# Kernel tuning notes

Hardware: AMD Instinct MI355X
Metric: run time of the kernel (lower is better)

Reference implementation:

```python
import jax, jax.numpy as jnp
import numpy as np

NUM_BANDS = 8
NUM_CHANNELS = 16
KC = NUM_BANDS * NUM_CHANNELS
EMA_KERNEL_LENGTH = 100
DELTA = 0.1
EPS = 1e-06
S_INIT = 0.04


def setup_inputs() -> dict:
    key = jax.random.key(0)
    kx, = jax.random.split(key, 1)
    x = jax.random.normal(kx, (32, NUM_BANDS, NUM_CHANNELS, 8192), dtype=jnp.float32)
    alpha_raw = jnp.zeros((KC,), dtype=jnp.float32)
    log_s = jnp.full((KC,), float(np.log(S_INIT / (1.0 - S_INIT))), dtype=jnp.float32)
    return {"x": x, "alpha_raw": alpha_raw, "log_s": log_s}


def _build_ema_kernel(log_s):
    # (KC, 1, L_full) causal EMA kernel, then caller slices last L taps
    Lf = EMA_KERNEL_LENGTH
    s = jax.nn.sigmoid(log_s)                      # (KC,)
    j = jnp.arange(Lf, dtype=s.dtype)              # (Lf,)
    impulse = s[:, None] * (1.0 - s[:, None]) ** j[None, :]   # (KC, Lf)
    impulse = impulse / (impulse.sum(axis=1, keepdims=True) + 1e-08)
    kernel = impulse[:, ::-1]                      # flip to causal conv kernel
    return kernel[:, None, :]                      # (KC, 1, Lf)


def reference(x, alpha_raw, log_s):
    B, K, C, T = x.shape
    x_flat = x.reshape(B, KC, T)
    alpha = jax.nn.sigmoid(alpha_raw) * 0.5        # (KC,) in (0, 0.5)
    x_mag = jnp.abs(x_flat)
    L = min(EMA_KERNEL_LENGTH, T)
    kernel = _build_ema_kernel(log_s)[:, :, -L:]   # (KC, 1, L)
    x_padded = jnp.pad(x_mag, ((0, 0), (0, 0), (L - 1, 0)))
    # depthwise causal conv: groups = KC
    M = jax.lax.conv_general_dilated(
        x_padded, kernel,
        window_strides=(1,), padding='VALID',
        feature_group_count=KC,
        dimension_numbers=('NCH', 'OIH', 'NCH'))   # (B, KC, T)
    gain = jnp.clip(M, EPS, None) ** alpha[None, :, None] + DELTA
    out_flat = x_flat / gain
    return out_flat.reshape(B, K, C, T)
```

## Files before the change

### kernel.cpp

```cpp
#include <hip/hip_runtime.h>
#include <math.h>


constexpr int T      = 8192;
constexpr int KC_    = 128;
constexpr int BLOCK  = 256;
constexpr int WPB    = BLOCK / 64;
constexpr int CHUNK  = 4;
constexpr int WELE   = 64 * CHUNK;
constexpr int WPR    = T / WELE;
constexpr int NHALO  = 25;
constexpr float EPS_   = 1e-6f;
constexpr float DELTA_ = 0.1f;
constexpr float LOG2E  = 1.4426950408889634f;

typedef float f32x4 __attribute__((ext_vector_type(4)));

__device__ __forceinline__ float fast_sigmoid(float x) {
    const float e = __builtin_amdgcn_exp2f(-x * LOG2E);
    return __builtin_amdgcn_rcpf(1.0f + e);
}

__device__ __forceinline__ float gain_div(float xv, float M, float alpha) {
    const float Mc = fmaxf(M, EPS_);
    const float g  = __builtin_amdgcn_exp2f(alpha * __builtin_amdgcn_logf(Mc)) + DELTA_;
    return xv * __builtin_amdgcn_rcpf(g);
}

__global__ __launch_bounds__(BLOCK, 8) void agc_kernel(
    const float* __restrict__ x,
    const float* __restrict__ alpha_raw,
    const float* __restrict__ log_s,
    float* __restrict__ out)
{
    __shared__ float Pe[WPB][92];

    const int tid  = threadIdx.x;
    const int lane = tid & 63;
    const int wv   = tid >> 6;
    const int gw   = blockIdx.x * WPB + wv;
    const int row  = gw / WPR;
    const int wrow = gw & (WPR - 1);
    const int kc   = row & (KC_ - 1);
    const float* __restrict__ xrow = x + (size_t)row * T;
    float* __restrict__ orow       = out + (size_t)row * T;
    const f32x4* __restrict__ x4   = reinterpret_cast<const f32x4*>(xrow);
    f32x4* __restrict__ o4         = reinterpret_cast<f32x4*>(orow);

    const int i4 = (wrow << 6) + lane;

    const f32x4 v = x4[i4];
    f32x4 pv = {0.0f, 0.0f, 0.0f, 0.0f};
    if (wrow != 0 || lane >= NHALO)
        pv = x4[i4 - NHALO];

    const float s     = fast_sigmoid(log_s[kc]);
    const float alpha = 0.5f * fast_sigmoid(alpha_raw[kc]);
    const float q     = 1.0f - s;
    const float lq    = __builtin_amdgcn_logf(q);
    const float q4    = (q * q) * (q * q);
    const float q8    = q4 * q4;
    const float q100  = __builtin_amdgcn_exp2f(100.0f * lq);
    const float norm  = (1.0f - q100) + 1e-8f;
    const float w0    = s / norm;
    const float c3    = w0 * q100;

    const float a0 = fabsf(v.x),  a1 = fabsf(v.y),  a2 = fabsf(v.z),  a3 = fabsf(v.w);
    const float b0 = fabsf(pv.x), b1 = fabsf(pv.y), b2 = fabsf(pv.z), b3 = fabsf(pv.w);

    const float pA = fmaf(q, fmaf(q, fmaf(q, a0, a1), a2), a3);
    const float pB = fmaf(q, fmaf(q, fmaf(q, b0, b1), b2), b3);

    Pe[wv][NHALO + lane] = pA;
    if (lane < NHALO) Pe[wv][lane] = pB;

    asm volatile("s_waitcnt lgkmcnt(0)" ::: "memory");

    float accE = Pe[wv][lane];
    float accO = Pe[wv][lane + 1];
    #pragma unroll
    for (int j = 2; j <= 24; j += 2) accE = fmaf(accE, q8, Pe[wv][lane + j]);
    #pragma unroll
    for (int j = 3; j <= 23; j += 2) accO = fmaf(accO, q8, Pe[wv][lane + j]);
    float M = w0 * fmaf(q4, accO, accE);

    f32x4 o;
    M = fmaf(q, M, fmaf(w0, a0, -c3 * b0));  o.x = gain_div(v.x, M, alpha);
    M = fmaf(q, M, fmaf(w0, a1, -c3 * b1));  o.y = gain_div(v.y, M, alpha);
    M = fmaf(q, M, fmaf(w0, a2, -c3 * b2));  o.z = gain_div(v.z, M, alpha);
    M = fmaf(q, M, fmaf(w0, a3, -c3 * b3));  o.w = gain_div(v.w, M, alpha);
    __builtin_nontemporal_store(o, &o4[i4]);
}

extern "C" void kernel_launch(void* const* d_in, const int* in_sizes, int n_in,
                              void* d_out, int out_size, void* d_ws, size_t ws_size,
                              hipStream_t stream) {
    const float* x         = (const float*)d_in[0];
    const float* alpha_raw = (const float*)d_in[1];
    const float* log_s     = (const float*)d_in[2];
    float* out             = (float*)d_out;
    const int nrows = in_sizes[0] / T;
    const int nblocks = nrows * (T / WELE) / WPB;
    agc_kernel<<<nblocks, BLOCK, 0, stream>>>(x, alpha_raw, log_s, out);
}
```

Baseline: 227.3 us.

## Precompute per-channel EMA constants in setup kernel and shuffle halo from registers

Adds a tiny setup kernel that computes the per-channel EMA coefficients once into workspace, so the main kernel loads them instead of recomputing sigmoid, log and exp per wave. Each lane now gets its previous-element data from a neighbouring lane through cross-lane shuffles, and only the first 25 lanes issue a second global load for the halo. This cuts redundant vector memory loads, at the cost of four shuffles per lane and an extra kernel launch with a dependency through workspace.

```diff
diff --git a/kernel.cpp b/kernel.cpp
--- a/kernel.cpp
+++ b/kernel.cpp
@@ -27,10 +27,31 @@
     return xv * __builtin_amdgcn_rcpf(g);
 }
 
+__global__ void agc_setup(const float* __restrict__ alpha_raw,
+                          const float* __restrict__ log_s,
+                          float* __restrict__ tab)
+{
+    const int kc = threadIdx.x;
+    const float s     = fast_sigmoid(log_s[kc]);
+    const float alpha = 0.5f * fast_sigmoid(alpha_raw[kc]);
+    const float q     = 1.0f - s;
+    const float lq    = __builtin_amdgcn_logf(q);
+    const float q4    = (q * q) * (q * q);
+    const float q8    = q4 * q4;
+    const float q100  = __builtin_amdgcn_exp2f(100.0f * lq);
+    const float norm  = (1.0f - q100) + 1e-8f;
+    const float w0    = s / norm;
+    const float c3    = w0 * q100;
+    f32x4* t = reinterpret_cast<f32x4*>(tab);
+    t[kc * 2]     = f32x4{q, alpha, w0, c3};
+    t[kc * 2 + 1] = f32x4{q4, q8, 0.0f, 0.0f};
+}
+
 __global__ __launch_bounds__(BLOCK, 8) void agc_kernel(
     const float* __restrict__ x,
     const float* __restrict__ alpha_raw,
     const float* __restrict__ log_s,
+    const float* __restrict__ tab,
     float* __restrict__ out)
 {
     __shared__ float Pe[WPB][92];
@@ -50,20 +71,35 @@
     const int i4 = (wrow << 6) + lane;
 
     const f32x4 v = x4[i4];
-    f32x4 pv = {0.0f, 0.0f, 0.0f, 0.0f};
-    if (wrow != 0 || lane >= NHALO)
-        pv = x4[i4 - NHALO];
+    f32x4 hl = {0.0f, 0.0f, 0.0f, 0.0f};
+    const bool halo_lane = (lane < NHALO);
+    if (halo_lane && wrow != 0)
+        hl = x4[i4 - NHALO];
 
-    const float s     = fast_sigmoid(log_s[kc]);
-    const float alpha = 0.5f * fast_sigmoid(alpha_raw[kc]);
-    const float q     = 1.0f - s;
-    const float lq    = __builtin_amdgcn_logf(q);
-    const float q4    = (q * q) * (q * q);
-    const float q8    = q4 * q4;
-    const float q100  = __builtin_amdgcn_exp2f(100.0f * lq);
-    const float norm  = (1.0f - q100) + 1e-8f;
-    const float w0    = s / norm;
-    const float c3    = w0 * q100;
+    float q, alpha, w0, c3, q4, q8;
+    if (tab != nullptr) {
+        const f32x4 c0 = reinterpret_cast<const f32x4*>(tab)[kc * 2];
+        const f32x4 c1 = reinterpret_cast<const f32x4*>(tab)[kc * 2 + 1];
+        q = c0.x; alpha = c0.y; w0 = c0.z; c3 = c0.w; q4 = c1.x; q8 = c1.y;
+    } else {
+        const float s  = fast_sigmoid(log_s[kc]);
+        alpha = 0.5f * fast_sigmoid(alpha_raw[kc]);
+        q = 1.0f - s;
+        const float lq   = __builtin_amdgcn_logf(q);
+        q4 = (q * q) * (q * q);
+        q8 = q4 * q4;
+        const float q100 = __builtin_amdgcn_exp2f(100.0f * lq);
+        const float norm = (1.0f - q100) + 1e-8f;
+        w0 = s / norm;
+        c3 = w0 * q100;
+    }
+
+    f32x4 pv;
+    pv.x = __shfl(v.x, lane - NHALO, 64);
+    pv.y = __shfl(v.y, lane - NHALO, 64);
+    pv.z = __shfl(v.z, lane - NHALO, 64);
+    pv.w = __shfl(v.w, lane - NHALO, 64);
+    if (halo_lane) pv = hl;
 
     const float a0 = fabsf(v.x),  a1 = fabsf(v.y),  a2 = fabsf(v.z),  a3 = fabsf(v.w);
     const float b0 = fabsf(pv.x), b1 = fabsf(pv.y), b2 = fabsf(pv.z), b3 = fabsf(pv.w);
@@ -72,7 +108,7 @@
     const float pB = fmaf(q, fmaf(q, fmaf(q, b0, b1), b2), b3);
 
     Pe[wv][NHALO + lane] = pA;
-    if (lane < NHALO) Pe[wv][lane] = pB;
+    if (halo_lane) Pe[wv][lane] = pB;
 
     asm volatile("s_waitcnt lgkmcnt(0)" ::: "memory");
 
@@ -101,5 +137,11 @@
     float* out             = (float*)d_out;
     const int nrows = in_sizes[0] / T;
     const int nblocks = nrows * (T / WELE) / WPB;
-    agc_kernel<<<nblocks, BLOCK, 0, stream>>>(x, alpha_raw, log_s, out);
+
+    float* tab = nullptr;
+    if (d_ws != nullptr && ws_size >= (size_t)(KC_ * 8 * sizeof(float))) {
+        tab = (float*)d_ws;
+        agc_setup<<<1, KC_, 0, stream>>>(alpha_raw, log_s, tab);
+    }
+    agc_kernel<<<nblocks, BLOCK, 0, stream>>>(x, alpha_raw, log_s, tab, out);
 }
```

Result: no change. 229.3 us (+0.9%).
